# Optimization experiments

Hardware: AMD Instinct MI355X
Metric: run time of the kernel (lower is better)

## Reference

```python
import jax, jax.numpy as jnp
import numpy as np

B, T, C, H = 2, 2048, 1024, 16
WINDOW = 512
SOFTCAP = 30.0


def setup_inputs() -> dict:
    key = jax.random.key(0)
    ks = jax.random.split(key, 4)
    s = 0.02
    return {
        "x": jax.random.normal(ks[0], (B, T, C), dtype=jnp.float32),
        "suffix_prefix_length": jax.random.randint(ks[1], (B,), 0, 256),
        "W_qkv": jax.random.normal(ks[2], (3 * C, C), dtype=jnp.float32) * s,
        "b_qkv": jnp.zeros((3 * C,), dtype=jnp.float32),
        "W_proj": jax.random.normal(ks[3], (C, C), dtype=jnp.float32) * s,
        "b_proj": jnp.zeros((C,), dtype=jnp.float32),
    }


def reference(x, suffix_prefix_length, W_qkv, b_qkv, W_proj, b_proj):
    Bb, Tt, Cc = x.shape
    d = Cc // H
    # fused qkv projection (torch Linear: x @ W.T + b)
    qkv = x @ W_qkv.T + b_qkv
    q, k, v = jnp.split(qkv, 3, axis=-1)
    q = q.reshape(Bb, Tt, H, d).transpose(0, 2, 1, 3)  # [B,H,T,d]
    k = k.reshape(Bb, Tt, H, d).transpose(0, 2, 1, 3)
    v = v.reshape(Bb, Tt, H, d).transpose(0, 2, 1, 3)

    scale = 1.0 / np.sqrt(d).astype(np.float32)
    scores = jnp.einsum("bhqd,bhkd->bhqk", q, k) * scale
    # tanh softcap applied to unmasked scores (flex_attention score_mod path)
    scores = jnp.tanh(scores / SOFTCAP) * SOFTCAP

    qi = jnp.arange(Tt)[:, None]
    kj = jnp.arange(Tt)[None, :]
    sliding_causal = (qi >= kj) & (qi - kj <= WINDOW)          # [T,T]
    prefix_global = kj[None, :, :] < suffix_prefix_length[:, None, None]  # [B,T,T]
    mask = sliding_causal[None, None, :, :] | prefix_global[:, None, :, :]

    scores = jnp.where(mask, scores, -jnp.inf)
    att = jax.nn.softmax(scores, axis=-1)
    y = jnp.einsum("bhqk,bhkd->bhqd", att, v)
    y = y.transpose(0, 2, 1, 3).reshape(Bb, Tt, Cc)
    return y @ W_proj.T + b_proj
```

## Files before the change

### kernel.cpp

```cpp
#include <hip/hip_runtime.h>
#include <hip/hip_bf16.h>

typedef __bf16 bf16x8 __attribute__((ext_vector_type(8)));
typedef float f32x4 __attribute__((ext_vector_type(4)));

#define DEVI __device__ __forceinline__

constexpr int B_ = 2, T_ = 2048, C_ = 1024, H_ = 16, D_ = 64;
constexpr int M_ = B_ * T_;
constexpr int K_ = C_;
constexpr int WINDOW_ = 512;
constexpr float SCALE_ = 0.125f;

DEVI unsigned short f2bf(float f) {
  return __builtin_bit_cast(unsigned short, (__bf16)f);
}

DEVI void gl_lds16(const unsigned short* g, unsigned short* l) {
  __builtin_amdgcn_global_load_lds(
      (const __attribute__((address_space(1))) unsigned int*)g,
      (__attribute__((address_space(3))) unsigned int*)l, 16, 0, 0);
}

__global__ void cvt_f32_bf16(const float* __restrict__ in,
                             unsigned short* __restrict__ out, int n4) {
  int i = blockIdx.x * blockDim.x + threadIdx.x;
  if (i >= n4) return;
  float4 v = reinterpret_cast<const float4*>(in)[i];
  ushort4 o;
  o.x = f2bf(v.x); o.y = f2bf(v.y); o.z = f2bf(v.z); o.w = f2bf(v.w);
  reinterpret_cast<ushort4*>(out)[i] = o;
}

template <int WHICH>
__global__ __launch_bounds__(256) void gemm_bt(
    const unsigned short* __restrict__ A, const unsigned short* __restrict__ W,
    const float* __restrict__ bias,
    unsigned short* __restrict__ oq, unsigned short* __restrict__ ok,
    unsigned short* __restrict__ ovt, float* __restrict__ of) {
  __shared__ alignas(16) unsigned short As[128 * 32];
  __shared__ alignas(16) unsigned short Bs[128 * 32];

  const int tid = threadIdx.x;
  const int n0 = blockIdx.x * 128, m0 = blockIdx.y * 128;
  const int lane = tid & 63, w = tid >> 6;
  const int wm = (w >> 1) * 64, wn = (w & 1) * 64;
  const int lr = lane & 15, lg = lane >> 4;
  const int srow = lane >> 2, scs = (lane & 3) << 3;

  f32x4 acc[4][4];
#pragma unroll
  for (int i = 0; i < 4; i++)
#pragma unroll
    for (int j = 0; j < 4; j++) acc[i][j] = f32x4{0.f, 0.f, 0.f, 0.f};

  for (int kt = 0; kt < K_; kt += 32) {
#pragma unroll
    for (int i = 0; i < 2; i++) {
      const int rb = i * 64 + w * 16;
      gl_lds16(&A[(size_t)(m0 + rb + srow) * K_ + kt + scs], &As[rb * 32]);
      gl_lds16(&W[(size_t)(n0 + rb + srow) * K_ + kt + scs], &Bs[rb * 32]);
    }
    __syncthreads();
    bf16x8 af[4], bf[4];
#pragma unroll
    for (int m = 0; m < 4; m++)
      af[m] = *reinterpret_cast<const bf16x8*>(&As[(wm + m * 16 + lr) * 32 + lg * 8]);
#pragma unroll
    for (int n = 0; n < 4; n++)
      bf[n] = *reinterpret_cast<const bf16x8*>(&Bs[(wn + n * 16 + lr) * 32 + lg * 8]);
#pragma unroll
    for (int m = 0; m < 4; m++)
#pragma unroll
      for (int n = 0; n < 4; n++)
        acc[m][n] = __builtin_amdgcn_mfma_f32_16x16x32_bf16(af[m], bf[n], acc[m][n], 0, 0, 0);
    __syncthreads();
  }

#pragma unroll
  for (int ms = 0; ms < 4; ms++) {
#pragma unroll
    for (int ns = 0; ns < 4; ns++) {
#pragma unroll
      for (int r = 0; r < 4; r++) {
        int m = m0 + wm + ms * 16 + lg * 4 + r;
        int n = n0 + wn + ns * 16 + lr;
        if constexpr (WHICH == 0) {
          float v = acc[ms][ns][r] + bias[n];
          int part = n >> 10, nc = n & 1023;
          int hh = nc >> 6, dd = nc & 63;
          int bb = m >> 11, tt = m & 2047;
          unsigned short bv = f2bf(v);
          if (part == 0)
            oq[(((size_t)(bb * H_ + hh)) * T_ + tt) * D_ + dd] = bv;
          else
            ok[(((size_t)(bb * H_ + hh)) * T_ + tt) * D_ + dd] = bv;
        } else if constexpr (WHICH == 1) {
          of[(size_t)m * C_ + n] = acc[ms][ns][r] + bias[n];
        } else {
          float v = acc[ms][ns][r] + bias[m];
          int hh = m >> 6, dd = m & 63;
          int bb = n >> 11, tt = n & 2047;
          ovt[(((size_t)(bb * H_ + hh)) * D_ + dd) * T_ + tt] = f2bf(v);
        }
      }
    }
  }
}

__global__ __launch_bounds__(256) void attn_fwd(
    const unsigned short* __restrict__ qg, const unsigned short* __restrict__ kg,
    const unsigned short* __restrict__ vtg, const int* __restrict__ spl_arr,
    unsigned short* __restrict__ out) {
  const int tid = threadIdx.x;
  const int l = tid & 63, w = tid >> 6;
  const int lr = l & 15, lg = l >> 4;

  constexpr float C1 = 0.012022458674074695f;
  constexpr float C3 = -86.56170245333781f;

  const int lin = blockIdx.x;
  const int xs = lin & 7, slot = lin >> 3;
  const int g = xs + 8 * (slot >> 5);
  const int iblk = slot & 31;
  const int b = g >> 4, h = g & 15;
  const int q_base = iblk * 64;
  const int i0 = q_base + w * 16;

  const int spl = spl_arr[b];
  const size_t bh = (size_t)(b * H_ + h);
  const unsigned short* qp = qg + bh * T_ * D_;
  const unsigned short* kp = kg + bh * T_ * D_;
  const unsigned short* vp = vtg + bh * (size_t)D_ * T_;

  __shared__ alignas(16) unsigned short Ks[64 * 64];
  __shared__ alignas(16) unsigned short Vs[64 * 64];
  __shared__ alignas(16) unsigned short Ps[4][16][80];

  bf16x8 aq0 = *reinterpret_cast<const bf16x8*>(qp + (size_t)(i0 + lr) * D_ + lg * 8);
  bf16x8 aq1 = *reinterpret_cast<const bf16x8*>(qp + (size_t)(i0 + lr) * D_ + 32 + lg * 8);

  const unsigned short one_bf = 0x3F80;
  bf16x8 ONES;
#pragma unroll
  for (int i = 0; i < 8; i++) ONES[i] = __builtin_bit_cast(__bf16, one_bf);

  f32x4 acc[4];
  f32x4 accl = f32x4{0.f, 0.f, 0.f, 0.f};
#pragma unroll
  for (int nb = 0; nb < 4; nb++) acc[nb] = f32x4{0.f, 0.f, 0.f, 0.f};

  const int pref_tiles = (spl + 63) >> 6;
  const int pref_end = pref_tiles << 6;
  int wl = q_base - WINDOW_; if (wl < 0) wl = 0; wl &= ~63;
  const int start2 = wl > pref_end ? wl : pref_end;
  const int hi = q_base + 63;
  const int n2 = (start2 <= hi) ? (((hi - start2) >> 6) + 1) : 0;
  const int ntot = pref_tiles + n2;

  const int strow = tid >> 2;
  const int c0 = (tid & 3) << 4;
  const int ssw = (strow & 7) << 3;

  for (int tb = 0; tb < ntot; tb++) {
    const int j0 = (tb < pref_tiles) ? (tb << 6) : (start2 + ((tb - pref_tiles) << 6));
    {
      const unsigned short* krow = kp + (size_t)(j0 + strow) * D_;
      const unsigned short* vrow = vp + (size_t)strow * T_ + j0;
      int4 ka0 = *reinterpret_cast<const int4*>(krow + c0);
      int4 ka1 = *reinterpret_cast<const int4*>(krow + c0 + 8);
      int4 va0 = *reinterpret_cast<const int4*>(vrow + c0);
      int4 va1 = *reinterpret_cast<const int4*>(vrow + c0 + 8);
      *reinterpret_cast<int4*>(&Ks[strow * 64 + (c0 ^ ssw)]) = ka0;
      *reinterpret_cast<int4*>(&Ks[strow * 64 + ((c0 + 8) ^ ssw)]) = ka1;
      *reinterpret_cast<int4*>(&Vs[strow * 64 + (c0 ^ ssw)]) = va0;
      *reinterpret_cast<int4*>(&Vs[strow * 64 + ((c0 + 8) ^ ssw)]) = va1;
    }
    __syncthreads();

    const bool rel = (j0 < spl) || (j0 + 63 >= i0 - WINDOW_ && j0 <= i0 + 15);
    if (rel) {
      f32x4 s[4];
#pragma unroll
      for (int ks = 0; ks < 4; ks++) {
        const int krow = ks * 16 + lr;
        const int sw = (krow & 7) << 3;
        bf16x8 b0 = *reinterpret_cast<const bf16x8*>(&Ks[krow * 64 + ((lg * 8) ^ sw)]);
        bf16x8 b1 = *reinterpret_cast<const bf16x8*>(&Ks[krow * 64 + ((32 + lg * 8) ^ sw)]);
        f32x4 t = f32x4{0.f, 0.f, 0.f, 0.f};
        t = __builtin_amdgcn_mfma_f32_16x16x32_bf16(aq0, b0, t, 0, 0, 0);
        s[ks] = __builtin_amdgcn_mfma_f32_16x16x32_bf16(aq1, b1, t, 0, 0, 0);
      }

      const bool fullv = (j0 + 63 < spl) ||
                         ((j0 + 63 <= i0) && (i0 + 15 - j0 <= WINDOW_));
      if (fullv) {
#pragma unroll
        for (int r = 0; r < 4; r++) {
          const int prow = lg * 4 + r;
#pragma unroll
          for (int ks = 0; ks < 4; ks++) {
            float t = __builtin_amdgcn_exp2f(s[ks][r] * C1);
            float p = __builtin_amdgcn_exp2f(C3 * __builtin_amdgcn_rcpf(1.0f + t));
            Ps[w][prow][ks * 16 + lr] = f2bf(p);
          }
        }
      } else {
#pragma unroll
        for (int r = 0; r < 4; r++) {
          const int prow = lg * 4 + r;
          const int irow = i0 + prow;
#pragma unroll
          for (int ks = 0; ks < 4; ks++) {
            const int jc = j0 + ks * 16 + lr;
            float t = __builtin_amdgcn_exp2f(s[ks][r] * C1);
            float p = __builtin_amdgcn_exp2f(C3 * __builtin_amdgcn_rcpf(1.0f + t));
            bool valid = (jc <= irow && irow - jc <= WINDOW_) || (jc < spl);
            p = valid ? p : 0.0f;
            Ps[w][prow][ks * 16 + lr] = f2bf(p);
          }
        }
      }

      asm volatile("s_waitcnt lgkmcnt(0)" ::: "memory");

      bf16x8 pa0 = *reinterpret_cast<const bf16x8*>(&Ps[w][lr][lg * 8]);
      bf16x8 pa1 = *reinterpret_cast<const bf16x8*>(&Ps[w][lr][32 + lg * 8]);

      accl = __builtin_amdgcn_mfma_f32_16x16x32_bf16(pa0, ONES, accl, 0, 0, 0);
      accl = __builtin_amdgcn_mfma_f32_16x16x32_bf16(pa1, ONES, accl, 0, 0, 0);

#pragma unroll
      for (int nb = 0; nb < 4; nb++) {
        const int vrow = nb * 16 + lr;
        const int sw = (vrow & 7) << 3;
        bf16x8 bv0 = *reinterpret_cast<const bf16x8*>(&Vs[vrow * 64 + ((lg * 8) ^ sw)]);
        bf16x8 bv1 = *reinterpret_cast<const bf16x8*>(&Vs[vrow * 64 + ((32 + lg * 8) ^ sw)]);
        acc[nb] = __builtin_amdgcn_mfma_f32_16x16x32_bf16(pa0, bv0, acc[nb], 0, 0, 0);
        acc[nb] = __builtin_amdgcn_mfma_f32_16x16x32_bf16(pa1, bv1, acc[nb], 0, 0, 0);
      }
    }
    __syncthreads();
  }

  float rl[4];
#pragma unroll
  for (int r = 0; r < 4; r++) rl[r] = __builtin_amdgcn_rcpf(accl[r]);
#pragma unroll
  for (int nb = 0; nb < 4; nb++) {
#pragma unroll
    for (int r = 0; r < 4; r++) {
      float o = acc[nb][r] * rl[r];
      int t = i0 + lg * 4 + r;
      out[((size_t)(b * T_ + t)) * C_ + h * D_ + nb * 16 + lr] = f2bf(o);
    }
  }
}

extern "C" void kernel_launch(void* const* d_in, const int* in_sizes, int n_in,
                              void* d_out, int out_size, void* d_ws, size_t ws_size,
                              hipStream_t stream) {
  const float* x = (const float*)d_in[0];
  const int* spl = (const int*)d_in[1];
  const float* Wqkv = (const float*)d_in[2];
  const float* bqkv = (const float*)d_in[3];
  const float* Wproj = (const float*)d_in[4];
  const float* bproj = (const float*)d_in[5];
  float* out = (float*)d_out;

  char* ws = (char*)d_ws;
  unsigned short* xb = (unsigned short*)ws;       ws += (size_t)M_ * K_ * 2;
  unsigned short* wqkvb = (unsigned short*)ws;    ws += (size_t)3 * C_ * K_ * 2;
  unsigned short* wprojb = (unsigned short*)ws;   ws += (size_t)C_ * K_ * 2;
  unsigned short* qb = (unsigned short*)ws;       ws += (size_t)M_ * C_ * 2;
  unsigned short* kb = (unsigned short*)ws;       ws += (size_t)M_ * C_ * 2;
  unsigned short* vtb = (unsigned short*)ws;      ws += (size_t)M_ * C_ * 2;
  unsigned short* ab = (unsigned short*)ws;       ws += (size_t)M_ * C_ * 2;

  {
    int n4 = (M_ * K_) / 4;
    cvt_f32_bf16<<<(n4 + 255) / 256, 256, 0, stream>>>(x, xb, n4);
  }
  {
    int n4 = (3 * C_ * K_) / 4;
    cvt_f32_bf16<<<(n4 + 255) / 256, 256, 0, stream>>>(Wqkv, wqkvb, n4);
  }
  {
    int n4 = (C_ * K_) / 4;
    cvt_f32_bf16<<<(n4 + 255) / 256, 256, 0, stream>>>(Wproj, wprojb, n4);
  }

  gemm_bt<0><<<dim3(2048 / 128, M_ / 128), 256, 0, stream>>>(
      xb, wqkvb, bqkv, qb, kb, nullptr, nullptr);

  gemm_bt<2><<<dim3(M_ / 128, 1024 / 128), 256, 0, stream>>>(
      wqkvb + (size_t)2048 * K_, xb, bqkv + 2048, nullptr, nullptr, vtb, nullptr);

  attn_fwd<<<dim3(1024), 256, 0, stream>>>(qb, kb, vtb, spl, ab);

  gemm_bt<1><<<dim3(C_ / 128, M_ / 128), 256, 0, stream>>>(
      ab, wprojb, bproj, nullptr, nullptr, nullptr, out);
}
```

Measured before the change: 191.0 us.

## Fuse conversions and QKV GEMMs; transpose V in LDS inside attention

Merges the three fp32-to-bf16 conversion launches into one kernel and merges the separate V-transposed GEMM into the single QKV GEMM. V is now stored in the same [B,H,T,D] layout as K and Q. The attention kernel transposes V into swizzled LDS through scalar 16-bit stores. This removes two launches and the strided transposed global writes of the V GEMM, at the cost of more, narrower LDS stores per tile in attention.

```diff
diff --git a/kernel.cpp b/kernel.cpp
--- a/kernel.cpp
+++ b/kernel.cpp
@@ -10,7 +10,6 @@
 constexpr int M_ = B_ * T_;
 constexpr int K_ = C_;
 constexpr int WINDOW_ = 512;
-constexpr float SCALE_ = 0.125f;
 
 DEVI unsigned short f2bf(float f) {
   return __builtin_bit_cast(unsigned short, (__bf16)f);
@@ -22,14 +21,24 @@
       (__attribute__((address_space(3))) unsigned int*)l, 16, 0, 0);
 }
 
-__global__ void cvt_f32_bf16(const float* __restrict__ in,
-                             unsigned short* __restrict__ out, int n4) {
+__global__ void cvt_all(const float* __restrict__ x, const float* __restrict__ wqkv,
+                        const float* __restrict__ wproj,
+                        unsigned short* __restrict__ xb,
+                        unsigned short* __restrict__ wqkvb,
+                        unsigned short* __restrict__ wprojb) {
+  constexpr int N1 = M_ * K_ / 4, N2 = 3 * C_ * K_ / 4, N3 = C_ * K_ / 4;
   int i = blockIdx.x * blockDim.x + threadIdx.x;
-  if (i >= n4) return;
-  float4 v = reinterpret_cast<const float4*>(in)[i];
+  const float* in;
+  unsigned short* out;
+  int idx;
+  if (i < N1) { in = x; out = xb; idx = i; }
+  else if (i < N1 + N2) { in = wqkv; out = wqkvb; idx = i - N1; }
+  else if (i < N1 + N2 + N3) { in = wproj; out = wprojb; idx = i - N1 - N2; }
+  else return;
+  float4 v = reinterpret_cast<const float4*>(in)[idx];
   ushort4 o;
   o.x = f2bf(v.x); o.y = f2bf(v.y); o.z = f2bf(v.z); o.w = f2bf(v.w);
-  reinterpret_cast<ushort4*>(out)[i] = o;
+  reinterpret_cast<ushort4*>(out)[idx] = o;
 }
 
 template <int WHICH>
@@ -37,7 +46,7 @@
     const unsigned short* __restrict__ A, const unsigned short* __restrict__ W,
     const float* __restrict__ bias,
     unsigned short* __restrict__ oq, unsigned short* __restrict__ ok,
-    unsigned short* __restrict__ ovt, float* __restrict__ of) {
+    unsigned short* __restrict__ ov, float* __restrict__ of) {
   __shared__ alignas(16) unsigned short As[128 * 32];
   __shared__ alignas(16) unsigned short Bs[128 * 32];
 
@@ -62,18 +71,18 @@
       gl_lds16(&W[(size_t)(n0 + rb + srow) * K_ + kt + scs], &Bs[rb * 32]);
     }
     __syncthreads();
-    bf16x8 af[4], bf[4];
+    bf16x8 af[4], bfr[4];
 #pragma unroll
     for (int m = 0; m < 4; m++)
       af[m] = *reinterpret_cast<const bf16x8*>(&As[(wm + m * 16 + lr) * 32 + lg * 8]);
 #pragma unroll
     for (int n = 0; n < 4; n++)
-      bf[n] = *reinterpret_cast<const bf16x8*>(&Bs[(wn + n * 16 + lr) * 32 + lg * 8]);
+      bfr[n] = *reinterpret_cast<const bf16x8*>(&Bs[(wn + n * 16 + lr) * 32 + lg * 8]);
 #pragma unroll
     for (int m = 0; m < 4; m++)
 #pragma unroll
       for (int n = 0; n < 4; n++)
-        acc[m][n] = __builtin_amdgcn_mfma_f32_16x16x32_bf16(af[m], bf[n], acc[m][n], 0, 0, 0);
+        acc[m][n] = __builtin_amdgcn_mfma_f32_16x16x32_bf16(af[m], bfr[n], acc[m][n], 0, 0, 0);
     __syncthreads();
   }
 
@@ -91,17 +100,12 @@
           int hh = nc >> 6, dd = nc & 63;
           int bb = m >> 11, tt = m & 2047;
           unsigned short bv = f2bf(v);
-          if (part == 0)
-            oq[(((size_t)(bb * H_ + hh)) * T_ + tt) * D_ + dd] = bv;
-          else
-            ok[(((size_t)(bb * H_ + hh)) * T_ + tt) * D_ + dd] = bv;
-        } else if constexpr (WHICH == 1) {
+          size_t addr = (((size_t)(bb * H_ + hh)) * T_ + tt) * D_ + dd;
+          if (part == 0) oq[addr] = bv;
+          else if (part == 1) ok[addr] = bv;
+          else ov[addr] = bv;
+        } else {
           of[(size_t)m * C_ + n] = acc[ms][ns][r] + bias[n];
-        } else {
-          float v = acc[ms][ns][r] + bias[m];
-          int hh = m >> 6, dd = m & 63;
-          int bb = n >> 11, tt = n & 2047;
-          ovt[(((size_t)(bb * H_ + hh)) * D_ + dd) * T_ + tt] = f2bf(v);
         }
       }
     }
@@ -110,7 +114,7 @@
 
 __global__ __launch_bounds__(256) void attn_fwd(
     const unsigned short* __restrict__ qg, const unsigned short* __restrict__ kg,
-    const unsigned short* __restrict__ vtg, const int* __restrict__ spl_arr,
+    const unsigned short* __restrict__ vg, const int* __restrict__ spl_arr,
     unsigned short* __restrict__ out) {
   const int tid = threadIdx.x;
   const int l = tid & 63, w = tid >> 6;
@@ -131,7 +135,7 @@
   const size_t bh = (size_t)(b * H_ + h);
   const unsigned short* qp = qg + bh * T_ * D_;
   const unsigned short* kp = kg + bh * T_ * D_;
-  const unsigned short* vp = vtg + bh * (size_t)D_ * T_;
+  const unsigned short* vp = vg + bh * T_ * D_;
 
   __shared__ alignas(16) unsigned short Ks[64 * 64];
   __shared__ alignas(16) unsigned short Vs[64 * 64];
@@ -166,15 +170,19 @@
     const int j0 = (tb < pref_tiles) ? (tb << 6) : (start2 + ((tb - pref_tiles) << 6));
     {
       const unsigned short* krow = kp + (size_t)(j0 + strow) * D_;
-      const unsigned short* vrow = vp + (size_t)strow * T_ + j0;
       int4 ka0 = *reinterpret_cast<const int4*>(krow + c0);
       int4 ka1 = *reinterpret_cast<const int4*>(krow + c0 + 8);
-      int4 va0 = *reinterpret_cast<const int4*>(vrow + c0);
-      int4 va1 = *reinterpret_cast<const int4*>(vrow + c0 + 8);
       *reinterpret_cast<int4*>(&Ks[strow * 64 + (c0 ^ ssw)]) = ka0;
       *reinterpret_cast<int4*>(&Ks[strow * 64 + ((c0 + 8) ^ ssw)]) = ka1;
-      *reinterpret_cast<int4*>(&Vs[strow * 64 + (c0 ^ ssw)]) = va0;
-      *reinterpret_cast<int4*>(&Vs[strow * 64 + ((c0 + 8) ^ ssw)]) = va1;
+      union { int4 v4[2]; unsigned short u[16]; } vv;
+      const unsigned short* vrow = vp + (size_t)(j0 + l) * D_ + w * 16;
+      vv.v4[0] = *reinterpret_cast<const int4*>(vrow);
+      vv.v4[1] = *reinterpret_cast<const int4*>(vrow + 8);
+#pragma unroll
+      for (int e = 0; e < 16; e++) {
+        const int d = w * 16 + e;
+        Vs[d * 64 + (l ^ ((d & 7) << 3))] = vv.u[e];
+      }
     }
     __syncthreads();
 
@@ -274,29 +282,18 @@
   unsigned short* wprojb = (unsigned short*)ws;   ws += (size_t)C_ * K_ * 2;
   unsigned short* qb = (unsigned short*)ws;       ws += (size_t)M_ * C_ * 2;
   unsigned short* kb = (unsigned short*)ws;       ws += (size_t)M_ * C_ * 2;
-  unsigned short* vtb = (unsigned short*)ws;      ws += (size_t)M_ * C_ * 2;
+  unsigned short* vb = (unsigned short*)ws;       ws += (size_t)M_ * C_ * 2;
   unsigned short* ab = (unsigned short*)ws;       ws += (size_t)M_ * C_ * 2;
 
   {
-    int n4 = (M_ * K_) / 4;
-    cvt_f32_bf16<<<(n4 + 255) / 256, 256, 0, stream>>>(x, xb, n4);
-  }
-  {
-    int n4 = (3 * C_ * K_) / 4;
-    cvt_f32_bf16<<<(n4 + 255) / 256, 256, 0, stream>>>(Wqkv, wqkvb, n4);
-  }
-  {
-    int n4 = (C_ * K_) / 4;
-    cvt_f32_bf16<<<(n4 + 255) / 256, 256, 0, stream>>>(Wproj, wprojb, n4);
-  }
-
-  gemm_bt<0><<<dim3(2048 / 128, M_ / 128), 256, 0, stream>>>(
-      xb, wqkvb, bqkv, qb, kb, nullptr, nullptr);
-
-  gemm_bt<2><<<dim3(M_ / 128, 1024 / 128), 256, 0, stream>>>(
-      wqkvb + (size_t)2048 * K_, xb, bqkv + 2048, nullptr, nullptr, vtb, nullptr);
-
-  attn_fwd<<<dim3(1024), 256, 0, stream>>>(qb, kb, vtb, spl, ab);
+    constexpr int NT = (M_ * K_ + 3 * C_ * K_ + C_ * K_) / 4;
+    cvt_all<<<(NT + 255) / 256, 256, 0, stream>>>(x, Wqkv, Wproj, xb, wqkvb, wprojb);
+  }
+
+  gemm_bt<0><<<dim3(3072 / 128, M_ / 128), 256, 0, stream>>>(
+      xb, wqkvb, bqkv, qb, kb, vb, nullptr);
+
+  attn_fwd<<<dim3(1024), 256, 0, stream>>>(qb, kb, vb, spl, ab);
 
   gemm_bt<1><<<dim3(C_ / 128, M_ / 128), 256, 0, stream>>>(
       ab, wprojb, bproj, nullptr, nullptr, nullptr, out);
```

New measurement: 178.2 us. -6.7%, faster.
